# Kernel tuning notes

Measured on AMD Instinct MI355X. Metric: run time of the kernel, lower is better.

## Reference

```python
import jax, jax.numpy as jnp
import numpy as np

B, N_DIM, K_DIM = 16384, 4096, 128


def setup_inputs() -> dict:
    key = jax.random.key(0)
    k1, k2, k3, k4 = jax.random.split(key, 4)
    x = jax.random.normal(k1, (B, N_DIM), dtype=jnp.float32)
    # nn.Linear(n_dim, 1): weight (1, n_dim), bias (1,)
    lim = 1.0 / np.sqrt(N_DIM)
    W = jax.random.uniform(k2, (1, N_DIM), dtype=jnp.float32, minval=-lim, maxval=lim)
    b = jax.random.uniform(k3, (1,), dtype=jnp.float32, minval=-lim, maxval=lim)
    # V initialized N(0, 0.001)
    V = 0.001 * jax.random.normal(k4, (N_DIM, K_DIM), dtype=jnp.float32)
    return {"x": x, "W": W, "b": b, "V": V}


def reference(x, W, b, V):
    # linear part: (B,1)
    linear = x @ W.T + b
    # term1 = 0.5 * sum_k (x @ V)_k^2  (torch code's 'sum_of_square')
    xv = x @ V  # (B, k)
    term1 = 0.5 * jnp.sum(xv * xv, axis=1, keepdims=True)
    # term2: torch's expand+matmul+bmm reduces algebraically to
    # -0.5 * (sum_i x_i)^2 * ||V.sum(0)||^2  (identical math, no (B,n,n) tensor)
    s = jnp.sum(V, axis=0)  # (k,)
    xsum = jnp.sum(x, axis=1, keepdims=True)  # (B,1)
    term2 = -0.5 * (xsum * xsum) * jnp.dot(s, s)
    return linear + term1 + term2
```

## Files before the change

### kernel.cpp

```cpp
#include <hip/hip_runtime.h>

typedef __bf16 bf16;
typedef __bf16 bf16x8 __attribute__((ext_vector_type(8)));
typedef float f32x16 __attribute__((ext_vector_type(16)));

#define B_ROWS 16384
#define N_DIM  4096
#define K_DIM  128

__global__ __launch_bounds__(256) void prep_kernel(const float* __restrict__ V,
                                                   float* __restrict__ spart,
                                                   bf16* __restrict__ Ut) {
    __shared__ bf16 tile[128 * 136];
    __shared__ float sp[256];
    const int t = threadIdx.x;
    const int jbase = blockIdx.x * 128;
    const int c  = t & 127;
    const int j0 = t >> 7;

    float sacc = 0.f;
#pragma unroll 8
    for (int i = 0; i < 64; ++i) {
        int j = j0 + 2 * i;
        float v = V[(size_t)(jbase + j) * K_DIM + c];
        sacc += v;
        tile[c * 136 + j] = (bf16)v;
    }
    sp[t] = sacc;
    __syncthreads();
    if (t < 128) spart[blockIdx.x * 128 + t] = sp[t] + sp[t + 128];

    const int col = t >> 1, half = t & 1;
#pragma unroll
    for (int i = 0; i < 4; ++i) {
        uint4 d = *(const uint4*)&tile[col * 136 + half * 64 + i * 16];
        *(uint4*)&Ut[(size_t)col * N_DIM + jbase + half * 64 + i * 16] = d;
    }
}

__global__ __launch_bounds__(256, 2) void fm_main(const float* __restrict__ x,
                                                  const float* __restrict__ W,
                                                  const float* __restrict__ bptr,
                                                  const bf16* __restrict__ Ut,
                                                  const float* __restrict__ spart,
                                                  float* __restrict__ out) {
    __shared__ __align__(16) char pool[81920];
    bf16* xs = (bf16*)pool;
    bf16* us = (bf16*)(pool + 16384);

    const int t    = threadIdx.x;
    const int wave = t >> 6;
    const int lane = t & 63;
    const int l31  = lane & 31;
    const int h    = lane >> 5;
    const int r0   = blockIdx.x * 32;

    const int srow = t >> 3;
    const int scg  = t & 7;

    f32x16 acc;
#pragma unroll
    for (int i = 0; i < 16; ++i) acc[i] = 0.f;

    float xsum_acc = 0.f, xw_acc = 0.f;
    const float* xrow = x + (size_t)(r0 + srow) * N_DIM + scg * 16;
    const float* wrow = W + scg * 16;
    const int dr = lane >> 4;
    const int dc = lane & 15;

    float4 a0 = *(const float4*)(xrow);
    float4 a1 = *(const float4*)(xrow + 4);
    float4 a2 = *(const float4*)(xrow + 8);
    float4 a3 = *(const float4*)(xrow + 12);
    float4 w0 = *(const float4*)(wrow);
    float4 w1 = *(const float4*)(wrow + 4);
    float4 w2 = *(const float4*)(wrow + 8);
    float4 w3 = *(const float4*)(wrow + 12);
    __builtin_amdgcn_sched_barrier(0);
#pragma unroll
    for (int j = 0; j < 8; ++j) {
        const int rw = j * 4 + dr;
        const bf16* src = Ut + (size_t)(wave * 32 + rw) * N_DIM
                             + (size_t)((dc ^ (rw & 15)) * 8);
        __builtin_amdgcn_global_load_lds(
            (const __attribute__((address_space(1))) void*)src,
            (__attribute__((address_space(3))) void*)&us[(wave * 32 + j * 4) * 128],
            16, 0, 0);
    }
    __builtin_amdgcn_sched_barrier(0);

#pragma unroll 2
    for (int it = 0; it < 32; ++it) {
        const int bsel = it & 1;
        const int kb1 = ((it < 31) ? (it + 1) : 0) * 128;

        bf16x8 xb;
        xb[0] = (bf16)a0.x; xb[1] = (bf16)a0.y; xb[2] = (bf16)a0.z; xb[3] = (bf16)a0.w;
        xb[4] = (bf16)a1.x; xb[5] = (bf16)a1.y; xb[6] = (bf16)a1.z; xb[7] = (bf16)a1.w;
        *(bf16x8*)&xs[bsel * 4096 + srow * 128 + (((scg * 2) ^ (srow & 15)) * 8)] = xb;
        xb[0] = (bf16)a2.x; xb[1] = (bf16)a2.y; xb[2] = (bf16)a2.z; xb[3] = (bf16)a2.w;
        xb[4] = (bf16)a3.x; xb[5] = (bf16)a3.y; xb[6] = (bf16)a3.z; xb[7] = (bf16)a3.w;
        *(bf16x8*)&xs[bsel * 4096 + srow * 128 + (((scg * 2 + 1) ^ (srow & 15)) * 8)] = xb;

        asm volatile("s_waitcnt lgkmcnt(0)" ::: "memory");
        __builtin_amdgcn_s_barrier();
        __builtin_amdgcn_sched_barrier(0);

        float4 n0 = *(const float4*)(xrow + kb1);
        float4 n1 = *(const float4*)(xrow + kb1 + 4);
        float4 n2 = *(const float4*)(xrow + kb1 + 8);
        float4 n3 = *(const float4*)(xrow + kb1 + 12);
        float4 m0 = *(const float4*)(wrow + kb1);
        float4 m1 = *(const float4*)(wrow + kb1 + 4);
        float4 m2 = *(const float4*)(wrow + kb1 + 8);
        float4 m3 = *(const float4*)(wrow + kb1 + 12);
        __builtin_amdgcn_sched_barrier(0);

#pragma unroll
        for (int j = 0; j < 8; ++j) {
            const int rw = j * 4 + dr;
            const bf16* src = Ut + (size_t)(wave * 32 + rw) * N_DIM + kb1
                                 + (size_t)((dc ^ (rw & 15)) * 8);
            __builtin_amdgcn_global_load_lds(
                (const __attribute__((address_space(1))) void*)src,
                (__attribute__((address_space(3))) void*)&us[(bsel ^ 1) * 16384 + (wave * 32 + j * 4) * 128],
                16, 0, 0);
        }
        __builtin_amdgcn_sched_barrier(0);

        xsum_acc += (a0.x + a0.y + a0.z + a0.w) + (a1.x + a1.y + a1.z + a1.w)
                  + (a2.x + a2.y + a2.z + a2.w) + (a3.x + a3.y + a3.z + a3.w);
        xw_acc   += a0.x * w0.x + a0.y * w0.y + a0.z * w0.z + a0.w * w0.w
                  + a1.x * w1.x + a1.y * w1.y + a1.z * w1.z + a1.w * w1.w
                  + a2.x * w2.x + a2.y * w2.y + a2.z * w2.z + a2.w * w2.w
                  + a3.x * w3.x + a3.y * w3.y + a3.z * w3.z + a3.w * w3.w;

        asm volatile("s_waitcnt vmcnt(16)" ::: "memory");
        __builtin_amdgcn_sched_barrier(0);

        __builtin_amdgcn_s_setprio(1);
#pragma unroll
        for (int ks = 0; ks < 128; ks += 16) {
            const int ch = (ks >> 3) + h;
            const int cx = (ch ^ (l31 & 15)) * 8;
            bf16x8 af  = *(const bf16x8*)&xs[bsel * 4096 + l31 * 128 + cx];
            bf16x8 bfv = *(const bf16x8*)&us[bsel * 16384 + (wave * 32 + l31) * 128 + cx];
            acc = __builtin_amdgcn_mfma_f32_32x32x16_bf16(af, bfv, acc, 0, 0, 0);
        }
        __builtin_amdgcn_s_setprio(0);

        a0 = n0; a1 = n1; a2 = n2; a3 = n3;
        w0 = m0; w1 = m1; w2 = m2; w3 = m3;
    }

    __syncthreads();
    float* redxs  = (float*)pool;
    float* redxw  = redxs + 256;
    float* rowsq  = redxw + 256;
    float* snred  = rowsq + 128;

    redxs[t] = xsum_acc;
    redxw[t] = xw_acc;

#pragma unroll
    for (int r = 0; r < 16; ++r) {
        float s = acc[r] * acc[r];
        s += __shfl_xor(s, 1);
        s += __shfl_xor(s, 2);
        s += __shfl_xor(s, 4);
        s += __shfl_xor(s, 8);
        s += __shfl_xor(s, 16);
        if (l31 == 0) {
            int row = (r & 3) + 8 * (r >> 2) + 4 * h;
            rowsq[wave * 32 + row] = s;
        }
    }

    if (t < 128) {
        float sv = 0.f;
#pragma unroll
        for (int bb = 0; bb < 32; ++bb) sv += spart[bb * 128 + t];
        float sq = sv * sv;
#pragma unroll
        for (int m = 32; m >= 1; m >>= 1) sq += __shfl_down(sq, m, 64);
        if ((t & 63) == 0) snred[t >> 6] = sq;
    }
    __syncthreads();

    if (t < 32) {
        float xsum = 0.f, xw = 0.f;
#pragma unroll
        for (int g = 0; g < 8; ++g) { xsum += redxs[t * 8 + g]; xw += redxw[t * 8 + g]; }
        float sq = rowsq[t] + rowsq[32 + t] + rowsq[64 + t] + rowsq[96 + t];
        float snorm = snred[0] + snred[1];
        float bv = bptr[0];
        out[r0 + t] = bv + xw + 0.5f * sq - 0.5f * xsum * xsum * snorm;
    }
}

extern "C" void kernel_launch(void* const* d_in, const int* in_sizes, int n_in,
                              void* d_out, int out_size, void* d_ws, size_t ws_size,
                              hipStream_t stream) {
    const float* x  = (const float*)d_in[0];
    const float* W  = (const float*)d_in[1];
    const float* bp = (const float*)d_in[2];
    const float* V  = (const float*)d_in[3];
    float* out = (float*)d_out;

    char* ws = (char*)d_ws;
    float* spart = (float*)(ws + 1024);
    bf16*  Ut    = (bf16*)(ws + 32768);

    hipLaunchKernelGGL(prep_kernel, dim3(32), dim3(256), 0, stream, V, spart, Ut);
    hipLaunchKernelGGL(fm_main, dim3(512), dim3(256), 0, stream, x, W, bp, Ut, spart, out);
}
```

Measured before the change: 371.6 us.

## Halve rows per block and split U staging into halves to raise occupancy

Each block now handles 16 rows instead of 32, launching 1024 blocks with 40KB LDS and a launch bound of four blocks per CU. The V-transposed buffer drops its full double buffer in favour of two 64-column halves, each refilled right after its MFMAs consume it. The goal is more resident waves and more parallelism to hide the memory-bound x stream. The cost is that half of each 32x32 MFMA tile is wasted on duplicated rows and the U tile is fetched from L2 twice as often per row.

```diff
diff --git a/kernel.cpp b/kernel.cpp
--- a/kernel.cpp
+++ b/kernel.cpp
@@ -38,54 +38,53 @@
     }
 }
 
-__global__ __launch_bounds__(256, 2) void fm_main(const float* __restrict__ x,
+__global__ __launch_bounds__(256, 4) void fm_main(const float* __restrict__ x,
                                                   const float* __restrict__ W,
                                                   const float* __restrict__ bptr,
                                                   const bf16* __restrict__ Ut,
                                                   const float* __restrict__ spart,
                                                   float* __restrict__ out) {
-    __shared__ __align__(16) char pool[81920];
+    __shared__ __align__(16) char pool[40960];
     bf16* xs = (bf16*)pool;
-    bf16* us = (bf16*)(pool + 16384);
+    bf16* us = (bf16*)(pool + 8192);
 
     const int t    = threadIdx.x;
     const int wave = t >> 6;
     const int lane = t & 63;
     const int l31  = lane & 31;
     const int h    = lane >> 5;
-    const int r0   = blockIdx.x * 32;
-
-    const int srow = t >> 3;
-    const int scg  = t & 7;
+    const int r0   = blockIdx.x * 16;
+
+    const int srow = t >> 4;
+    const int scg  = t & 15;
 
     f32x16 acc;
 #pragma unroll
     for (int i = 0; i < 16; ++i) acc[i] = 0.f;
 
     float xsum_acc = 0.f, xw_acc = 0.f;
-    const float* xrow = x + (size_t)(r0 + srow) * N_DIM + scg * 16;
-    const float* wrow = W + scg * 16;
-    const int dr = lane >> 4;
-    const int dc = lane & 15;
+    const float* xrow = x + (size_t)(r0 + srow) * N_DIM + scg * 8;
+    const float* wrow = W + scg * 8;
+    const int drw = lane >> 3;
+    const int dch = lane & 7;
 
     float4 a0 = *(const float4*)(xrow);
     float4 a1 = *(const float4*)(xrow + 4);
-    float4 a2 = *(const float4*)(xrow + 8);
-    float4 a3 = *(const float4*)(xrow + 12);
     float4 w0 = *(const float4*)(wrow);
     float4 w1 = *(const float4*)(wrow + 4);
-    float4 w2 = *(const float4*)(wrow + 8);
-    float4 w3 = *(const float4*)(wrow + 12);
     __builtin_amdgcn_sched_barrier(0);
 #pragma unroll
-    for (int j = 0; j < 8; ++j) {
-        const int rw = j * 4 + dr;
-        const bf16* src = Ut + (size_t)(wave * 32 + rw) * N_DIM
-                             + (size_t)((dc ^ (rw & 15)) * 8);
-        __builtin_amdgcn_global_load_lds(
-            (const __attribute__((address_space(1))) void*)src,
-            (__attribute__((address_space(3))) void*)&us[(wave * 32 + j * 4) * 128],
-            16, 0, 0);
+    for (int hs = 0; hs < 2; ++hs) {
+#pragma unroll
+        for (int j = 0; j < 4; ++j) {
+            const int rw = j * 8 + drw;
+            const bf16* src = Ut + (size_t)(wave * 32 + rw) * N_DIM + hs * 64
+                                 + (size_t)((dch ^ (rw & 7)) * 8);
+            __builtin_amdgcn_global_load_lds(
+                (const __attribute__((address_space(1))) void*)src,
+                (__attribute__((address_space(3))) void*)&us[hs * 8192 + (wave * 32 + j * 8) * 64],
+                16, 0, 0);
+        }
     }
     __builtin_amdgcn_sched_barrier(0);
 
@@ -97,10 +96,7 @@
         bf16x8 xb;
         xb[0] = (bf16)a0.x; xb[1] = (bf16)a0.y; xb[2] = (bf16)a0.z; xb[3] = (bf16)a0.w;
         xb[4] = (bf16)a1.x; xb[5] = (bf16)a1.y; xb[6] = (bf16)a1.z; xb[7] = (bf16)a1.w;
-        *(bf16x8*)&xs[bsel * 4096 + srow * 128 + (((scg * 2) ^ (srow & 15)) * 8)] = xb;
-        xb[0] = (bf16)a2.x; xb[1] = (bf16)a2.y; xb[2] = (bf16)a2.z; xb[3] = (bf16)a2.w;
-        xb[4] = (bf16)a3.x; xb[5] = (bf16)a3.y; xb[6] = (bf16)a3.z; xb[7] = (bf16)a3.w;
-        *(bf16x8*)&xs[bsel * 4096 + srow * 128 + (((scg * 2 + 1) ^ (srow & 15)) * 8)] = xb;
+        *(bf16x8*)&xs[bsel * 2048 + srow * 128 + ((scg ^ srow) * 8)] = xb;
 
         asm volatile("s_waitcnt lgkmcnt(0)" ::: "memory");
         __builtin_amdgcn_s_barrier();
@@ -108,62 +104,78 @@
 
         float4 n0 = *(const float4*)(xrow + kb1);
         float4 n1 = *(const float4*)(xrow + kb1 + 4);
-        float4 n2 = *(const float4*)(xrow + kb1 + 8);
-        float4 n3 = *(const float4*)(xrow + kb1 + 12);
         float4 m0 = *(const float4*)(wrow + kb1);
         float4 m1 = *(const float4*)(wrow + kb1 + 4);
-        float4 m2 = *(const float4*)(wrow + kb1 + 8);
-        float4 m3 = *(const float4*)(wrow + kb1 + 12);
-        __builtin_amdgcn_sched_barrier(0);
-
-#pragma unroll
-        for (int j = 0; j < 8; ++j) {
-            const int rw = j * 4 + dr;
+        __builtin_amdgcn_sched_barrier(0);
+
+        xsum_acc += (a0.x + a0.y + a0.z + a0.w) + (a1.x + a1.y + a1.z + a1.w);
+        xw_acc   += a0.x * w0.x + a0.y * w0.y + a0.z * w0.z + a0.w * w0.w
+                  + a1.x * w1.x + a1.y * w1.y + a1.z * w1.z + a1.w * w1.w;
+        __builtin_amdgcn_sched_barrier(0);
+
+        asm volatile("s_waitcnt vmcnt(8)" ::: "memory");
+        __builtin_amdgcn_sched_barrier(0);
+        __builtin_amdgcn_s_setprio(1);
+#pragma unroll
+        for (int ks = 0; ks < 64; ks += 16) {
+            const int ch = (ks >> 3) + h;
+            bf16x8 af  = *(const bf16x8*)&xs[bsel * 2048 + (l31 & 15) * 128 + ((ch ^ (l31 & 15)) * 8)];
+            bf16x8 bfv = *(const bf16x8*)&us[(wave * 32 + l31) * 64 + ((ch ^ (l31 & 7)) * 8)];
+            acc = __builtin_amdgcn_mfma_f32_32x32x16_bf16(af, bfv, acc, 0, 0, 0);
+        }
+        __builtin_amdgcn_s_setprio(0);
+        __builtin_amdgcn_sched_barrier(0);
+#pragma unroll
+        for (int j = 0; j < 4; ++j) {
+            const int rw = j * 8 + drw;
             const bf16* src = Ut + (size_t)(wave * 32 + rw) * N_DIM + kb1
-                                 + (size_t)((dc ^ (rw & 15)) * 8);
+                                 + (size_t)((dch ^ (rw & 7)) * 8);
             __builtin_amdgcn_global_load_lds(
                 (const __attribute__((address_space(1))) void*)src,
-                (__attribute__((address_space(3))) void*)&us[(bsel ^ 1) * 16384 + (wave * 32 + j * 4) * 128],
+                (__attribute__((address_space(3))) void*)&us[(wave * 32 + j * 8) * 64],
                 16, 0, 0);
         }
         __builtin_amdgcn_sched_barrier(0);
 
-        xsum_acc += (a0.x + a0.y + a0.z + a0.w) + (a1.x + a1.y + a1.z + a1.w)
-                  + (a2.x + a2.y + a2.z + a2.w) + (a3.x + a3.y + a3.z + a3.w);
-        xw_acc   += a0.x * w0.x + a0.y * w0.y + a0.z * w0.z + a0.w * w0.w
-                  + a1.x * w1.x + a1.y * w1.y + a1.z * w1.z + a1.w * w1.w
-                  + a2.x * w2.x + a2.y * w2.y + a2.z * w2.z + a2.w * w2.w
-                  + a3.x * w3.x + a3.y * w3.y + a3.z * w3.z + a3.w * w3.w;
-
-        asm volatile("s_waitcnt vmcnt(16)" ::: "memory");
-        __builtin_amdgcn_sched_barrier(0);
-
+        asm volatile("s_waitcnt vmcnt(8)" ::: "memory");
+        __builtin_amdgcn_sched_barrier(0);
         __builtin_amdgcn_s_setprio(1);
 #pragma unroll
-        for (int ks = 0; ks < 128; ks += 16) {
+        for (int ks = 64; ks < 128; ks += 16) {
             const int ch = (ks >> 3) + h;
-            const int cx = (ch ^ (l31 & 15)) * 8;
-            bf16x8 af  = *(const bf16x8*)&xs[bsel * 4096 + l31 * 128 + cx];
-            bf16x8 bfv = *(const bf16x8*)&us[bsel * 16384 + (wave * 32 + l31) * 128 + cx];
+            const int c8 = ch & 7;
+            bf16x8 af  = *(const bf16x8*)&xs[bsel * 2048 + (l31 & 15) * 128 + ((ch ^ (l31 & 15)) * 8)];
+            bf16x8 bfv = *(const bf16x8*)&us[8192 + (wave * 32 + l31) * 64 + ((c8 ^ (l31 & 7)) * 8)];
             acc = __builtin_amdgcn_mfma_f32_32x32x16_bf16(af, bfv, acc, 0, 0, 0);
         }
         __builtin_amdgcn_s_setprio(0);
-
-        a0 = n0; a1 = n1; a2 = n2; a3 = n3;
-        w0 = m0; w1 = m1; w2 = m2; w3 = m3;
+        __builtin_amdgcn_sched_barrier(0);
+#pragma unroll
+        for (int j = 0; j < 4; ++j) {
+            const int rw = j * 8 + drw;
+            const bf16* src = Ut + (size_t)(wave * 32 + rw) * N_DIM + kb1 + 64
+                                 + (size_t)((dch ^ (rw & 7)) * 8);
+            __builtin_amdgcn_global_load_lds(
+                (const __attribute__((address_space(1))) void*)src,
+                (__attribute__((address_space(3))) void*)&us[8192 + (wave * 32 + j * 8) * 64],
+                16, 0, 0);
+        }
+        __builtin_amdgcn_sched_barrier(0);
+
+        a0 = n0; a1 = n1; w0 = m0; w1 = m1;
     }
 
     __syncthreads();
     float* redxs  = (float*)pool;
     float* redxw  = redxs + 256;
     float* rowsq  = redxw + 256;
-    float* snred  = rowsq + 128;
+    float* snred  = rowsq + 64;
 
     redxs[t] = xsum_acc;
     redxw[t] = xw_acc;
 
 #pragma unroll
-    for (int r = 0; r < 16; ++r) {
+    for (int r = 0; r < 8; ++r) {
         float s = acc[r] * acc[r];
         s += __shfl_xor(s, 1);
         s += __shfl_xor(s, 2);
@@ -172,7 +184,7 @@
         s += __shfl_xor(s, 16);
         if (l31 == 0) {
             int row = (r & 3) + 8 * (r >> 2) + 4 * h;
-            rowsq[wave * 32 + row] = s;
+            rowsq[wave * 16 + row] = s;
         }
     }
 
@@ -187,11 +199,11 @@
     }
     __syncthreads();
 
-    if (t < 32) {
+    if (t < 16) {
         float xsum = 0.f, xw = 0.f;
 #pragma unroll
-        for (int g = 0; g < 8; ++g) { xsum += redxs[t * 8 + g]; xw += redxw[t * 8 + g]; }
-        float sq = rowsq[t] + rowsq[32 + t] + rowsq[64 + t] + rowsq[96 + t];
+        for (int g = 0; g < 16; ++g) { xsum += redxs[t * 16 + g]; xw += redxw[t * 16 + g]; }
+        float sq = rowsq[t] + rowsq[16 + t] + rowsq[32 + t] + rowsq[48 + t];
         float snorm = snred[0] + snred[1];
         float bv = bptr[0];
         out[r0 + t] = bv + xw + 0.5f * sq - 0.5f * xsum * xsum * snorm;
@@ -212,5 +224,5 @@
     bf16*  Ut    = (bf16*)(ws + 32768);
 
     hipLaunchKernelGGL(prep_kernel, dim3(32), dim3(256), 0, stream, V, spart, Ut);
-    hipLaunchKernelGGL(fm_main, dim3(512), dim3(256), 0, stream, x, W, bp, Ut, spart, out);
+    hipLaunchKernelGGL(fm_main, dim3(1024), dim3(256), 0, stream, x, W, bp, Ut, spart, out);
 }
```

Measured after the change: 383.7 us. 1.03x slower.
